# Kernel tuning notes

Measured on AMD Instinct MI355X. Metric: run time of the kernel, lower is better.

Reference implementation:

```python
import jax, jax.numpy as jnp
import numpy as np

B, T, C = 2, 2048, 4096
NH, NKV, HD = 32, 8, 128
GROUPS = NH // NKV
THETA = 10000.0


def _rope_tables(seq_len, dim, theta, dtype):
    inv_freq = 1.0 / (theta ** (jnp.arange(0, dim, 2, dtype=jnp.float32) / dim))
    t = jnp.arange(seq_len, dtype=jnp.float32)
    freqs = jnp.outer(t, inv_freq)            # [T, dim/2]
    emb = jnp.concatenate([freqs, freqs], -1)  # [T, dim]
    return jnp.cos(emb).astype(dtype), jnp.sin(emb).astype(dtype)


def _rotate_half(x):
    h = x.shape[-1] // 2
    return jnp.concatenate([-x[..., h:], x[..., :h]], axis=-1)


def setup_inputs() -> dict:
    key = jax.random.key(0)
    ks = jax.random.split(key, 5)
    s = 1.0 / np.sqrt(C)
    return {
        "x": jax.random.normal(ks[0], (B, T, C), jnp.float32),
        "wq": jax.random.normal(ks[1], (C, NH * HD), jnp.float32) * s,
        "wk": jax.random.normal(ks[2], (C, NKV * HD), jnp.float32) * s,
        "wv": jax.random.normal(ks[3], (C, NKV * HD), jnp.float32) * s,
        "wo": jax.random.normal(ks[4], (NH * HD, C), jnp.float32) * s,
    }


def reference(x, wq, wk, wv, wo):
    b, t, c = x.shape
    q = (x @ wq).reshape(b, t, NH, HD).transpose(0, 2, 1, 3)    # [B,NH,T,HD]
    k = (x @ wk).reshape(b, t, NKV, HD).transpose(0, 2, 1, 3)   # [B,NKV,T,HD]
    v = (x @ wv).reshape(b, t, NKV, HD).transpose(0, 2, 1, 3)
    cos, sin = _rope_tables(t, HD, THETA, x.dtype)              # [T,HD]
    cos = cos[None, None]
    sin = sin[None, None]
    q = q * cos + _rotate_half(q) * sin
    k = k * cos + _rotate_half(k) * sin
    # GQA: broadcast KV heads over groups via einsum instead of materializing repeat
    qg = q.reshape(b, NKV, GROUPS, t, HD)
    scores = jnp.einsum('bkgqd,bkld->bkgql', qg, k) * (HD ** -0.5)  # [B,NKV,G,T,T]
    causal = jnp.triu(jnp.full((t, t), -jnp.inf, dtype=x.dtype), k=1)
    scores = scores + causal
    attn = jax.nn.softmax(scores, axis=-1)
    out = jnp.einsum('bkgql,bkld->bkgqd', attn, v)              # [B,NKV,G,T,HD]
    out = out.reshape(b, NH, t, HD).transpose(0, 2, 1, 3).reshape(b, t, NH * HD)
    return out @ wo
```

## Files before the change

kernel.cpp:

```cpp
#include <hip/hip_runtime.h>
#include <hip/hip_bf16.h>
#include <math.h>

#define B_ 2
#define T_ 2048
#define C_ 4096
#define NH_ 32
#define NKV_ 8
#define HD_ 128
#define M_ (B_*T_)
#define QKVN_ (NH_*HD_ + 2*NKV_*HD_)

using bf16 = __hip_bfloat16;
typedef __bf16 bf16x8 __attribute__((ext_vector_type(8)));
typedef float f32x4 __attribute__((ext_vector_type(4)));

__device__ inline f32x4 mfma16(bf16x8 a, bf16x8 b, f32x4 c) {
    return __builtin_amdgcn_mfma_f32_16x16x32_bf16(a, b, c, 0, 0, 0);
}

__global__ __launch_bounds__(256) void cast_f32_bf16(const float* __restrict__ in,
                                                     bf16* __restrict__ out, int n4) {
    int i = blockIdx.x * 256 + threadIdx.x;
    if (i >= n4) return;
    float4 v = reinterpret_cast<const float4*>(in)[i];
    union { bf16 h[4]; uint2 u; } o;
    o.h[0] = __float2bfloat16(v.x);
    o.h[1] = __float2bfloat16(v.y);
    o.h[2] = __float2bfloat16(v.z);
    o.h[3] = __float2bfloat16(v.w);
    reinterpret_cast<uint2*>(out)[i] = o.u;
}

__global__ __launch_bounds__(256) void transpose_cast(const float* __restrict__ in,
                                                      bf16* __restrict__ out, int K, int N) {
    __shared__ float tile[32][33];
    int tx = threadIdx.x & 31, ty = threadIdx.x >> 5;
    int n0 = blockIdx.x << 5, k0 = blockIdx.y << 5;
#pragma unroll
    for (int p = 0; p < 4; ++p)
        tile[p*8 + ty][tx] = in[(size_t)(k0 + p*8 + ty) * N + n0 + tx];
    __syncthreads();
#pragma unroll
    for (int p = 0; p < 4; ++p)
        out[(size_t)(n0 + p*8 + ty) * K + k0 + tx] = __float2bfloat16(tile[tx][p*8 + ty]);
}

__global__ __launch_bounds__(256) void rope_tab(float2* __restrict__ tab) {
    int idx = blockIdx.x * 256 + threadIdx.x;
    int i = idx & 63, t = idx >> 6;
    float inv = exp2f((float)i * -0.20762050593045952f);
    float th = (float)t * inv;
    tab[idx] = make_float2(cosf(th), sinf(th));
}

#define GEMM_PROLOG_AND_LOOP(TAG)                                                       \
    f32x4 acc[8][4] = {};                                                               \
    bf16x8 a[4][2], b0[2][2], b1[2][2];                                                 \
    STAGE_HALF(Ag, 0,     0, 0, 0); STAGE_HALF(Ag, 0,     0, 0, 1);                     \
    STAGE_HALF(Bg, 65536, 0, 0, 0); STAGE_HALF(Bg, 65536, 0, 0, 1);                     \
    STAGE_HALF(Bg, 65536, 1, 1, 0); STAGE_HALF(Bg, 65536, 1, 1, 1);                     \
    asm volatile("s_waitcnt vmcnt(4)" ::: "memory");                                    \
    BAR();                                                                              \
    for (int it = 0; it < (nt >> 1); ++it) {                                            \
        const int u = 2 * it;                                                           \
        const bool more = (u + 2) < nt;                                                 \
        const bool more3 = (u + 3) < nt;                                                \
        READ_A(0, 0); READ_B(0, 0, b0);                                                 \
        STAGE_HALF(Ag, 0, u + 1, 1, 0);                                                 \
        MFMA_Q(0, 0, b0);                                                               \
        BAR();                                                                          \
        READ_B(0, 1, b1);                                                               \
        STAGE_HALF(Ag, 0, u + 1, 1, 1);                                                 \
        MFMA_Q(0, 2, b1);                                                               \
        BAR();                                                                          \
        READ_A(0, 1);                                                                   \
        if (more) STAGE_HALF(Bg, 65536, u + 2, 0, 0);                                   \
        MFMA_Q(4, 2, b1);                                                               \
        BAR();                                                                          \
        if (more) STAGE_HALF(Bg, 65536, u + 2, 0, 1);                                   \
        MFMA_Q(4, 0, b0);                                                               \
        if (more) asm volatile("s_waitcnt vmcnt(8)" ::: "memory");                      \
        else      asm volatile("s_waitcnt vmcnt(4)" ::: "memory");                      \
        BAR();                                                                          \
        READ_A(1, 0); READ_B(1, 0, b0);                                                 \
        if (more) STAGE_HALF(Ag, 0, u + 2, 0, 0);                                       \
        MFMA_Q(0, 0, b0);                                                               \
        BAR();                                                                          \
        READ_B(1, 1, b1);                                                               \
        if (more) STAGE_HALF(Ag, 0, u + 2, 0, 1);                                       \
        MFMA_Q(0, 2, b1);                                                               \
        if (more) asm volatile("s_waitcnt vmcnt(8)" ::: "memory");                      \
        else      asm volatile("s_waitcnt vmcnt(0)" ::: "memory");                      \
        BAR();                                                                          \
        READ_A(1, 1);                                                                   \
        if (more3) STAGE_HALF(Bg, 65536, u + 3, 1, 0);                                  \
        MFMA_Q(4, 2, b1);                                                               \
        BAR();                                                                          \
        if (more3) STAGE_HALF(Bg, 65536, u + 3, 1, 1);                                  \
        MFMA_Q(4, 0, b0);                                                               \
        if (more3) asm volatile("s_waitcnt vmcnt(4)" ::: "memory");                     \
        else       asm volatile("s_waitcnt vmcnt(0)" ::: "memory");                     \
        BAR();                                                                          \
    }

#define GEMM_COMMON_DEFS                                                                \
    __shared__ __align__(16) char lds[131072];                                          \
    const int tid = threadIdx.x;                                                        \
    const int wid = tid >> 6, lane = tid & 63;                                          \
    const int lq = lane & 15, lg = lane >> 4;                                           \
    const int wrow = wid >> 2, wcol = wid & 3;                                          \
    const int nwg = gridDim.x;                                                          \
    const int q8 = nwg >> 3;                                                            \
    const int wg = (blockIdx.x & 7) * q8 + (blockIdx.x >> 3);                           \
    const int nby = M >> 8;                                                             \
    const int by = wg % nby, bx = wg / nby;                                             \
    const int brow = by << 8, bcol = bx << 8;                                           \
    const bf16* Ag = A + (size_t)brow * K;                                              \
    const bf16* Bg = Bt + (size_t)bcol * K;                                             \
    const int nt = K >> 6;                                                              \
    const int srow = (wid << 3) + (lane >> 3);                                          \
    const int schunk = (lane & 7) ^ ((lane >> 3) & 7);

#define STAGE_HALF(gbase, ldsoff, t2, cbuf, hf)                                         \
    {                                                                                   \
        _Pragma("unroll")                                                               \
        for (int l = 0; l < 2; ++l) {                                                   \
            const int r0 = (hf) * 128 + l * 64;                                         \
            const char* src = (const char*)(gbase) +                                    \
                ((size_t)(r0 + srow) * K + (size_t)(t2) * 64) * 2 + schunk * 16;        \
            char* dst = &lds[(ldsoff) + (cbuf) * 32768 + (r0 + (wid << 3)) * 128];      \
            __builtin_amdgcn_global_load_lds(                                           \
                (const __attribute__((address_space(1))) void*)src,                     \
                (__attribute__((address_space(3))) void*)dst, 16, 0, 0);                \
        }                                                                               \
    }

#define LDA(cbuf, mh, mf, ks) \
    (*(const bf16x8*)&lds[(cbuf)*32768 + (wrow*128 + (mh)*64 + (mf)*16 + lq)*128 + ((((ks)*4 + lg)) ^ (lq & 7))*16])

#define READ_A(cbuf, mh) \
    { _Pragma("unroll") for (int mf = 0; mf < 4; ++mf) { a[mf][0] = LDA(cbuf, mh, mf, 0); a[mf][1] = LDA(cbuf, mh, mf, 1); } }
#define READ_B(cbuf, nh, breg) \
    { _Pragma("unroll") for (int nf = 0; nf < 2; ++nf) { breg[nf][0] = LDB(cbuf, nh, nf, 0); breg[nf][1] = LDB(cbuf, nh, nf, 1); } }
#define MFMA_Q(am, an, breg)                                                     \
    { __builtin_amdgcn_s_setprio(1);                                             \
      _Pragma("unroll") for (int mf = 0; mf < 4; ++mf)                           \
          _Pragma("unroll") for (int nf = 0; nf < 2; ++nf)                       \
              _Pragma("unroll") for (int ks = 0; ks < 2; ++ks)                   \
                  acc[(am) + mf][(an) + nf] = mfma16(a[mf][ks], breg[nf][ks],    \
                                                     acc[(am) + mf][(an) + nf]); \
      __builtin_amdgcn_s_setprio(0); }
#define BAR() __builtin_amdgcn_s_barrier()

__device__ inline void store_out(float* p, float v) { *p = v; }
__device__ inline void store_out(bf16*  p, float v) { *p = __float2bfloat16(v); }

template <typename OutT>
__global__ __launch_bounds__(512, 2) void gemm256(const bf16* __restrict__ A,
                                                  const bf16* __restrict__ Bt,
                                                  OutT* __restrict__ C,
                                                  int M, int N, int K) {
    GEMM_COMMON_DEFS
#define LDB(cbuf, nh, nf, ks) \
    (*(const bf16x8*)&lds[65536 + (cbuf)*32768 + (wcol*64 + (nh)*32 + (nf)*16 + lq)*128 + ((((ks)*4 + lg)) ^ (lq & 7))*16])
    GEMM_PROLOG_AND_LOOP(plain)
#undef LDB
#pragma unroll
    for (int mf = 0; mf < 8; ++mf)
#pragma unroll
        for (int nf = 0; nf < 4; ++nf)
#pragma unroll
            for (int r = 0; r < 4; ++r) {
                int row = brow + wrow * 128 + mf * 16 + lg * 4 + r;
                int col = bcol + wcol * 64 + nf * 16 + lq;
                store_out(&C[(size_t)row * N + col], acc[mf][nf][r]);
            }
}

__global__ __launch_bounds__(512, 2) void gemm_qkv(const bf16* __restrict__ A,
                                                   const bf16* __restrict__ Bt,
                                                   bf16* __restrict__ q_r,
                                                   const float2* __restrict__ tab,
                                                   int M, int K) {
    GEMM_COMMON_DEFS
#define LDB(cbuf, nh, nf, ks) \
    (*(const bf16x8*)&lds[65536 + (cbuf)*32768 + (((wcol>>1)*128 + (wcol&1)*32 + (nh)*64 + (nf)*16 + lq))*128 + ((((ks)*4 + lg)) ^ (lq & 7))*16])
    GEMM_PROLOG_AND_LOOP(remap)
#undef LDB

    const int trow = brow + wrow * 128;
    const float sc = 0.12751741230963214f;
#pragma unroll
    for (int mf = 0; mf < 8; ++mf)
#pragma unroll
        for (int j = 0; j < 2; ++j)
#pragma unroll
            for (int r = 0; r < 4; ++r) {
                int row = trow + mf*16 + lg*4 + r;
                int bb = row >> 11, tt = row & 2047;
                int i  = (wcol&1)*32 + j*16 + lq;
                float2 cs = tab[tt*64 + i];
                float x0 = acc[mf][j][r], x1 = acc[mf][j+2][r];
                float y0 = (x0*cs.x - x1*cs.y) * sc;
                float y1 = (x1*cs.x + x0*cs.y) * sc;
                int col0 = bcol + (wcol>>1)*128 + i;
                int h = col0 >> 7, hd = col0 & 127;
                bf16* dst = q_r + ((size_t)(bb*NH_ + h)*T_ + tt)*HD_;
                dst[hd]      = __float2bfloat16(y0);
                dst[hd + 64] = __float2bfloat16(y1);
            }
}

#undef GEMM_PROLOG_AND_LOOP
#undef GEMM_COMMON_DEFS
#undef STAGE_HALF
#undef LDA
#undef READ_A
#undef READ_B
#undef MFMA_Q
#undef BAR

__global__ __launch_bounds__(512, 2) void gemm_kv(const bf16* __restrict__ A,
                                                  const bf16* __restrict__ BtKV,
                                                  bf16* __restrict__ k_r,
                                                  bf16* __restrict__ vbuf,
                                                  const float2* __restrict__ tab,
                                                  int M, int K) {
    __shared__ __align__(16) char lds[98304];
    const int tid = threadIdx.x;
    const int wid = tid >> 6, lane = tid & 63;
    const int lq = lane & 15, lg = lane >> 4;
    const int wrow = wid >> 2, wcol = wid & 3;

    const int nwg = gridDim.x;
    const int q8 = nwg >> 3;
    const int wg = (blockIdx.x & 7) * q8 + (blockIdx.x >> 3);
    const int nby = M >> 7;
    const int by = wg % nby, bx = wg / nby;
    const int brow = by << 7;
    const int bcolr = bx << 8;

    const bf16* Ag = A + (size_t)brow * K;
    const bf16* Bg = BtKV + (size_t)bcolr * K;
    const int nt = K >> 6;

    const int srow = (wid << 3) + (lane >> 3);
    const int schunk = (lane & 7) ^ ((lane >> 3) & 7);

#define KV_STAGE_A(t2, cbuf, hf)                                                        \
    {                                                                                   \
        const char* src = (const char*)Ag +                                             \
            ((size_t)((hf) * 64 + srow) * K + (size_t)(t2) * 64) * 2 + schunk * 16;     \
        char* dst = &lds[(cbuf) * 16384 + ((hf) * 64 + (wid << 3)) * 128];              \
        __builtin_amdgcn_global_load_lds(                                               \
            (const __attribute__((address_space(1))) void*)src,                         \
            (__attribute__((address_space(3))) void*)dst, 16, 0, 0);                    \
    }
#define KV_STAGE_B(t2, cbuf, hf)                                                        \
    {                                                                                   \
        _Pragma("unroll")                                                               \
        for (int l = 0; l < 2; ++l) {                                                   \
            const int r0 = (hf) * 128 + l * 64;                                         \
            const char* src = (const char*)Bg +                                         \
                ((size_t)(r0 + srow) * K + (size_t)(t2) * 64) * 2 + schunk * 16;        \
            char* dst = &lds[32768 + (cbuf) * 32768 + (r0 + (wid << 3)) * 128];         \
            __builtin_amdgcn_global_load_lds(                                           \
                (const __attribute__((address_space(1))) void*)src,                     \
                (__attribute__((address_space(3))) void*)dst, 16, 0, 0);                \
        }                                                                               \
    }
#define KV_LDA(cbuf, mh, f, ks) \
    (*(const bf16x8*)&lds[(cbuf)*16384 + (wrow*64 + (mh)*32 + (f)*16 + lq)*128 + ((((ks)*4 + lg)) ^ (lq & 7))*16])
#define KV_LDB(cbuf, nh, nf, ks) \
    (*(const bf16x8*)&lds[32768 + (cbuf)*32768 + (((wcol>>1)*128 + (wcol&1)*32 + (nh)*64 + (nf)*16 + lq))*128 + ((((ks)*4 + lg)) ^ (lq & 7))*16])
#define KV_READ_A(cbuf, mh) \
    { _Pragma("unroll") for (int f = 0; f < 2; ++f) { a[f][0] = KV_LDA(cbuf, mh, f, 0); a[f][1] = KV_LDA(cbuf, mh, f, 1); } }
#define KV_READ_B(cbuf, nh, breg) \
    { _Pragma("unroll") for (int nf = 0; nf < 2; ++nf) { breg[nf][0] = KV_LDB(cbuf, nh, nf, 0); breg[nf][1] = KV_LDB(cbuf, nh, nf, 1); } }
#define KV_MFMA(am, an, breg)                                                    \
    { __builtin_amdgcn_s_setprio(1);                                             \
      _Pragma("unroll") for (int f = 0; f < 2; ++f)                              \
          _Pragma("unroll") for (int nf = 0; nf < 2; ++nf)                       \
              _Pragma("unroll") for (int ks = 0; ks < 2; ++ks)                   \
                  acc[(am) + f][(an) + nf] = mfma16(a[f][ks], breg[nf][ks],      \
                                                    acc[(am) + f][(an) + nf]);   \
      __builtin_amdgcn_s_setprio(0); }
#define KV_BAR() __builtin_amdgcn_s_barrier()

    f32x4 acc[4][4] = {};
    bf16x8 a[2][2], b0[2][2], b1[2][2];

    KV_STAGE_A(0, 0, 0); KV_STAGE_A(0, 0, 1);
    KV_STAGE_B(0, 0, 0); KV_STAGE_B(0, 0, 1);
    KV_STAGE_B(1, 1, 0); KV_STAGE_B(1, 1, 1);
    asm volatile("s_waitcnt vmcnt(4)" ::: "memory");
    KV_BAR();

    for (int it = 0; it < (nt >> 1); ++it) {
        const int u = 2 * it;
        const bool more = (u + 2) < nt;
        const bool more3 = (u + 3) < nt;

        KV_READ_A(0, 0); KV_READ_B(0, 0, b0);
        KV_STAGE_A(u + 1, 1, 0);
        KV_MFMA(0, 0, b0);
        KV_BAR();
        KV_READ_B(0, 1, b1);
        KV_STAGE_A(u + 1, 1, 1);
        KV_MFMA(0, 2, b1);
        KV_BAR();
        KV_READ_A(0, 1);
        if (more) KV_STAGE_B(u + 2, 0, 0);
        KV_MFMA(2, 2, b1);
        KV_BAR();
        if (more) KV_STAGE_B(u + 2, 0, 1);
        KV_MFMA(2, 0, b0);
        if (more) asm volatile("s_waitcnt vmcnt(4)" ::: "memory");
        else      asm volatile("s_waitcnt vmcnt(0)" ::: "memory");
        KV_BAR();
        KV_READ_A(1, 0); KV_READ_B(1, 0, b0);
        if (more) KV_STAGE_A(u + 2, 0, 0);
        KV_MFMA(0, 0, b0);
        KV_BAR();
        KV_READ_B(1, 1, b1);
        if (more) KV_STAGE_A(u + 2, 0, 1);
        KV_MFMA(0, 2, b1);
        KV_BAR();
        KV_READ_A(1, 1);
        if (more3) KV_STAGE_B(u + 3, 1, 0);
        KV_MFMA(2, 2, b1);
        KV_BAR();
        if (more3) KV_STAGE_B(u + 3, 1, 1);
        KV_MFMA(2, 0, b0);
        if (more3) asm volatile("s_waitcnt vmcnt(4)" ::: "memory");
        else       asm volatile("s_waitcnt vmcnt(0)" ::: "memory");
        KV_BAR();
    }

    const int trow = brow + wrow * 64;
    if (bcolr >= 1024) {
#pragma unroll
        for (int mf = 0; mf < 4; ++mf)
#pragma unroll
            for (int j = 0; j < 4; ++j)
#pragma unroll
                for (int r = 0; r < 4; ++r) {
                    int row = trow + (mf>>1)*32 + (mf&1)*16 + lg*4 + r;
                    int col = bcolr + (wcol>>1)*128 + (wcol&1)*32 + (j>>1)*64 + (j&1)*16 + lq - 1024;
                    vbuf[(size_t)row * (NKV_*HD_) + col] = __float2bfloat16(acc[mf][j][r]);
                }
    } else {
#pragma unroll
        for (int mf = 0; mf < 4; ++mf)
#pragma unroll
            for (int j = 0; j < 2; ++j)
#pragma unroll
                for (int r = 0; r < 4; ++r) {
                    int row = trow + (mf>>1)*32 + (mf&1)*16 + lg*4 + r;
                    int bb = row >> 11, tt = row & 2047;
                    int i  = (wcol&1)*32 + j*16 + lq;
                    float2 cs = tab[tt*64 + i];
                    float x0 = acc[mf][j][r], x1 = acc[mf][j+2][r];
                    float y0 = x0*cs.x - x1*cs.y;
                    float y1 = x1*cs.x + x0*cs.y;
                    int col0 = bcolr + (wcol>>1)*128 + i;
                    int h = col0 >> 7, hd = col0 & 127;
                    bf16* dst = k_r + ((size_t)(bb*NKV_ + h)*T_ + tt)*HD_;
                    dst[hd]      = __float2bfloat16(y0);
                    dst[hd + 64] = __float2bfloat16(y1);
                }
    }
#undef KV_STAGE_A
#undef KV_STAGE_B
#undef KV_LDA
#undef KV_LDB
#undef KV_READ_A
#undef KV_READ_B
#undef KV_MFMA
#undef KV_BAR
}

__global__ __launch_bounds__(256) void vtrans(const bf16* __restrict__ vbuf,
                                              bf16* __restrict__ vt) {
    __shared__ bf16 tile[32][33];
    int gx = blockIdx.x;
    int dt = gx & 3;
    int tt = (gx >> 2) & 63;
    int kv = (gx >> 8) & 7;
    int b  = gx >> 11;
    int d0 = dt * 32, t0 = tt * 32;
    int tx = threadIdx.x & 31, ty = threadIdx.x >> 5;

    const bf16* src = vbuf + (size_t)(b * T_ + t0) * (NKV_*HD_) + kv * HD_ + d0;
#pragma unroll
    for (int p = 0; p < 4; ++p)
        tile[p*8 + ty][tx] = src[(size_t)(p*8 + ty) * (NKV_*HD_) + tx];
    __syncthreads();
    bf16* dst = vt + ((size_t)((b * NKV_ + kv) * HD_ + d0)) * T_ + t0;
#pragma unroll
    for (int p = 0; p < 4; ++p)
        dst[(size_t)(p*8 + ty) * T_ + tx] = tile[tx][p*8 + ty];
}

__global__ __launch_bounds__(1024) void fattn(const bf16* __restrict__ Q,
                                              const bf16* __restrict__ Kt,
                                              const bf16* __restrict__ VT,
                                              bf16* __restrict__ O) {
    const int lin = blockIdx.x;
    const int kv = lin & 7;
    const int b  = (lin >> 3) & 1;
    const int idx = lin >> 4;
    const int h  = kv * 4 + (idx & 3);
    const int jp = idx >> 2;

    const int tid = threadIdx.x, wid = tid >> 6, lane = tid & 63;
    const int lq = lane & 15, lg = lane >> 4;

    const bf16* Kp = Kt + (size_t)(b * NKV_ + kv) * T_ * HD_;
    const bf16* Vp = VT + (size_t)(b * NKV_ + kv) * HD_ * T_;

    __shared__ __align__(16) bf16 Ks[2][64][128];
    __shared__ __align__(16) bf16 Vs[2][128][64];
    __shared__ __align__(16) bf16 p_lds[16][16][72];

    const float THR_L2 = 11.5416f;

#define STAGE_KV(cbuf, tt)                                                           \
    { {                                                                              \
        int krow = wid * 4 + (lane >> 4);                                            \
        int kch  = (lane & 15) ^ (krow & 15);                                        \
        const bf16* ksrc = Kp + (size_t)((tt) * 64 + krow) * HD_ + kch * 8;          \
        __builtin_amdgcn_global_load_lds(                                            \
            (const __attribute__((address_space(1))) void*)ksrc,                     \
            (__attribute__((address_space(3))) void*)&Ks[cbuf][wid*4][0],            \
            16, 0, 0);                                                               \
      }                                                                              \
      {                                                                              \
        int vrow = wid * 8 + (lane >> 3);                                            \
        int vch  = (lane & 7) ^ (vrow & 7);                                          \
        const bf16* vsrc = Vp + (size_t)vrow * T_ + (tt) * 64 + vch * 8;             \
        __builtin_amdgcn_global_load_lds(                                            \
            (const __attribute__((address_space(1))) void*)vsrc,                     \
            (__attribute__((address_space(3))) void*)&Vs[cbuf][wid*8][0],            \
            16, 0, 0);                                                               \
      } }

    for (int half = 0; half < 2; ++half) {
        const int qt = half ? (7 - jp) : jp;
        const int q0 = qt * 256 + wid * 16;
        const int kv_end = q0 + 16;
        const int NT = qt * 4 + 4;

        const bf16* Qp = Q + ((size_t)(b * NH_ + h) * T_ + q0) * HD_;
        bf16x8 qf[4];
#pragma unroll
        for (int c = 0; c < 4; ++c)
            qf[c] = *(const bf16x8*)&Qp[(size_t)lq * HD_ + c * 32 + lg * 8];

        f32x4 oacc[8] = {};
        float m_r = -INFINITY;
        float l_r = 0.f;

        STAGE_KV(0, 0);
        STAGE_KV(1, 1);
        asm volatile("s_waitcnt vmcnt(2)" ::: "memory");
        __builtin_amdgcn_s_barrier();

        for (int t = 0; t < NT; ++t) {
            const int cb = t & 1;
            const int t0 = t * 64;

            if (t0 < kv_end) {
                f32x4 st[4] = {};
#pragma unroll
                for (int n = 0; n < 4; ++n) {
                    bf16x8 kf[4];
#pragma unroll
                    for (int c = 0; c < 4; ++c)
                        kf[c] = *(const bf16x8*)((const char*)&Ks[cb][n*16 + lq][0]
                                                  + (((c*4 + lg) ^ lq) << 4));
                    __builtin_amdgcn_s_setprio(1);
#pragma unroll
                    for (int c = 0; c < 4; ++c)
                        st[n] = mfma16(kf[c], qf[c], st[n]);
                    __builtin_amdgcn_s_setprio(0);
                }

                const int qq = q0 + lq;
#pragma unroll
                for (int n = 0; n < 4; ++n)
#pragma unroll
                    for (int r = 0; r < 4; ++r) {
                        int kk = t0 + n*16 + lg*4 + r;
                        if (kk > qq) st[n][r] = -INFINITY;
                    }

                float rmax = st[0][0];
#pragma unroll
                for (int n = 0; n < 4; ++n)
#pragma unroll
                    for (int r = 0; r < 4; ++r) rmax = fmaxf(rmax, st[n][r]);
                rmax = fmaxf(rmax, __shfl_xor(rmax, 16));
                rmax = fmaxf(rmax, __shfl_xor(rmax, 32));

                if (__any(rmax - m_r > THR_L2)) {
                    float mnew = fmaxf(m_r, rmax);
                    float alpha = exp2f(m_r - mnew);
                    m_r = mnew;
                    l_r *= alpha;
#pragma unroll
                    for (int r = 0; r < 4; ++r) {
                        float a_pv = __shfl(alpha, lg*4 + r);
#pragma unroll
                        for (int f = 0; f < 8; ++f) oacc[f][r] *= a_pv;
                    }
                }

                float rsum = 0.f;
#pragma unroll
                for (int n = 0; n < 4; ++n)
#pragma unroll
                    for (int r = 0; r < 4; ++r) {
                        float p = exp2f(st[n][r] - m_r);
                        st[n][r] = p;
                        rsum += p;
                    }
                rsum += __shfl_xor(rsum, 16);
                rsum += __shfl_xor(rsum, 32);
                l_r += rsum;

#pragma unroll
                for (int n = 0; n < 4; ++n) {
                    union { bf16 hh[4]; uint2 u; } pk;
#pragma unroll
                    for (int r = 0; r < 4; ++r) pk.hh[r] = __float2bfloat16(st[n][r]);
                    *(uint2*)&p_lds[wid][lq][n*16 + lg*4] = pk.u;
                }

#pragma unroll
                for (int ks = 0; ks < 2; ++ks) {
                    bf16x8 pa = *(const bf16x8*)&p_lds[wid][lq][ks*32 + lg*8];
                    bf16x8 vf[8];
#pragma unroll
                    for (int f = 0; f < 8; ++f)
                        vf[f] = *(const bf16x8*)((const char*)&Vs[cb][f*16 + lq][0]
                                                  + (((ks*4 + lg) ^ (lq & 7)) << 4));
                    __builtin_amdgcn_s_setprio(1);
#pragma unroll
                    for (int f = 0; f < 8; ++f)
                        oacc[f] = mfma16(pa, vf[f], oacc[f]);
                    __builtin_amdgcn_s_setprio(0);
                }
            }

            __builtin_amdgcn_s_barrier();
            if (t + 2 < NT) {
                STAGE_KV(cb, t + 2);
                asm volatile("s_waitcnt vmcnt(2)" ::: "memory");
            } else {
                asm volatile("s_waitcnt vmcnt(0)" ::: "memory");
            }
            __builtin_amdgcn_s_barrier();
        }

        {
            float rinv = __builtin_amdgcn_rcpf(l_r);
#pragma unroll
            for (int r = 0; r < 4; ++r) {
                float rl = __shfl(rinv, lg*4 + r);
                int row = q0 + lg*4 + r;
#pragma unroll
                for (int f = 0; f < 8; ++f) {
                    int d = f*16 + lq;
                    O[((size_t)(b * T_ + row) * NH_ + h) * HD_ + d] =
                        __float2bfloat16(oacc[f][r] * rl);
                }
            }
        }
    }
#undef STAGE_KV
}

extern "C" void kernel_launch(void* const* d_in, const int* in_sizes, int n_in,
                              void* d_out, int out_size, void* d_ws, size_t ws_size,
                              hipStream_t stream) {
    const float* x  = (const float*)d_in[0];
    const float* wq = (const float*)d_in[1];
    const float* wk = (const float*)d_in[2];
    const float* wv = (const float*)d_in[3];
    const float* wo = (const float*)d_in[4];
    float* out = (float*)d_out;

    bf16* ws    = (bf16*)d_ws;
    bf16* xb    = ws;
    bf16* wqkvT = xb + (size_t)M_ * C_;
    bf16* qr_wo = wqkvT + (size_t)QKVN_ * C_;
    bf16* region = qr_wo + (size_t)C_ * C_;
    bf16* k_r  = region;
    bf16* vt   = k_r + (size_t)B_ * NKV_ * T_ * HD_;
    bf16* vbuf = vt  + (size_t)B_ * NKV_ * T_ * HD_;
    float2* tab = (float2*)(vbuf + (size_t)B_ * T_ * NKV_ * HD_);

    bf16* attn = xb;

    cast_f32_bf16<<<(M_ * C_ / 4 + 255) / 256, 256, 0, stream>>>(x, xb, M_ * C_ / 4);
    transpose_cast<<<dim3(128, 128), 256, 0, stream>>>(wq, wqkvT, C_, NH_ * HD_);
    transpose_cast<<<dim3(32, 128), 256, 0, stream>>>(wk, wqkvT + (size_t)(NH_ * HD_) * C_, C_, NKV_ * HD_);
    transpose_cast<<<dim3(32, 128), 256, 0, stream>>>(wv, wqkvT + (size_t)(NH_ * HD_ + NKV_ * HD_) * C_, C_, NKV_ * HD_);
    rope_tab<<<(T_ * 64) / 256, 256, 0, stream>>>(tab);

    gemm_qkv<<<dim3((C_ / 256) * (M_ / 256)), 512, 0, stream>>>(
        xb, wqkvT, qr_wo, tab, M_, C_);
    gemm_kv<<<dim3(256), 512, 0, stream>>>(
        xb, wqkvT + (size_t)(NH_ * HD_) * C_, k_r, vbuf, tab, M_, C_);

    vtrans<<<B_ * NKV_ * (T_ / 32) * (HD_ / 32), 256, 0, stream>>>(vbuf, vt);

    fattn<<<dim3(256), 1024, 0, stream>>>(qr_wo, k_r, vt, attn);

    transpose_cast<<<dim3(128, 128), 256, 0, stream>>>(wo, qr_wo, NH_ * HD_, C_);
    gemm256<float><<<dim3((C_ / 256) * (M_ / 256)), 512, 0, stream>>>(attn, qr_wo, out, M_, C_, C_);
}
```

Measured before the change: 478.1 us.

## Merge Q and KV projection GEMMs into one kernel and fuse weight transposes

Combines the three QKV weight transpose-cast launches into a single kernel that picks the source matrix by block index. Also fuses the Q projection GEMM and the KV projection GEMM into one 256-block kernel where each workgroup first computes a Q tile, then a KV tile, sharing one LDS allocation. This removes launch overhead and the tail/idle gap between the two GEMMs, at the cost of serializing both tiles per block and a fixed grid size that must match both tilings.

After: 471.5 us. About the same (-1.4%).

```diff
diff --git a/kernel.cpp b/kernel.cpp
--- a/kernel.cpp
+++ b/kernel.cpp
@@ -44,6 +44,27 @@
 #pragma unroll
     for (int p = 0; p < 4; ++p)
         out[(size_t)(n0 + p*8 + ty) * K + k0 + tx] = __float2bfloat16(tile[tx][p*8 + ty]);
+}
+
+__global__ __launch_bounds__(256) void transpose_cast3(const float* __restrict__ wq,
+                                                       const float* __restrict__ wk,
+                                                       const float* __restrict__ wv,
+                                                       bf16* __restrict__ out, int K) {
+    __shared__ float tile[32][33];
+    int tx = threadIdx.x & 31, ty = threadIdx.x >> 5;
+    int nt = blockIdx.x, k0 = blockIdx.y << 5;
+    const float* src; int N, nloc;
+    if (nt < 128)      { src = wq; N = 4096; nloc = nt << 5; }
+    else if (nt < 160) { src = wk; N = 1024; nloc = (nt - 128) << 5; }
+    else               { src = wv; N = 1024; nloc = (nt - 160) << 5; }
+#pragma unroll
+    for (int p = 0; p < 4; ++p)
+        tile[p*8 + ty][tx] = src[(size_t)(k0 + p*8 + ty) * N + nloc + tx];
+    __syncthreads();
+    int nglob = nt << 5;
+#pragma unroll
+    for (int p = 0; p < 4; ++p)
+        out[(size_t)(nglob + p*8 + ty) * K + k0 + tx] = __float2bfloat16(tile[tx][p*8 + ty]);
 }
 
 __global__ __launch_bounds__(256) void rope_tab(float2* __restrict__ tab) {
@@ -105,7 +126,6 @@
     }
 
 #define GEMM_COMMON_DEFS                                                                \
-    __shared__ __align__(16) char lds[131072];                                          \
     const int tid = threadIdx.x;                                                        \
     const int wid = tid >> 6, lane = tid & 63;                                          \
     const int lq = lane & 15, lg = lane >> 4;                                           \
@@ -113,12 +133,6 @@
     const int nwg = gridDim.x;                                                          \
     const int q8 = nwg >> 3;                                                            \
     const int wg = (blockIdx.x & 7) * q8 + (blockIdx.x >> 3);                           \
-    const int nby = M >> 8;                                                             \
-    const int by = wg % nby, bx = wg / nby;                                             \
-    const int brow = by << 8, bcol = bx << 8;                                           \
-    const bf16* Ag = A + (size_t)brow * K;                                              \
-    const bf16* Bg = Bt + (size_t)bcol * K;                                             \
-    const int nt = K >> 6;                                                              \
     const int srow = (wid << 3) + (lane >> 3);                                          \
     const int schunk = (lane & 7) ^ ((lane >> 3) & 7);
 
@@ -161,7 +175,14 @@
                                                   const bf16* __restrict__ Bt,
                                                   OutT* __restrict__ C,
                                                   int M, int N, int K) {
+    __shared__ __align__(16) char lds[131072];
     GEMM_COMMON_DEFS
+    const int nby = M >> 8;
+    const int by = wg % nby, bx = wg / nby;
+    const int brow = by << 8, bcol = bx << 8;
+    const bf16* Ag = A + (size_t)brow * K;
+    const bf16* Bg = Bt + (size_t)bcol * K;
+    const int nt = K >> 6;
 #define LDB(cbuf, nh, nf, ks) \
     (*(const bf16x8*)&lds[65536 + (cbuf)*32768 + (wcol*64 + (nh)*32 + (nf)*16 + lq)*128 + ((((ks)*4 + lg)) ^ (lq & 7))*16])
     GEMM_PROLOG_AND_LOOP(plain)
@@ -178,75 +199,59 @@
             }
 }
 
-__global__ __launch_bounds__(512, 2) void gemm_qkv(const bf16* __restrict__ A,
-                                                   const bf16* __restrict__ Bt,
-                                                   bf16* __restrict__ q_r,
-                                                   const float2* __restrict__ tab,
-                                                   int M, int K) {
+__global__ __launch_bounds__(512, 2) void gemm_qkv_all(const bf16* __restrict__ A,
+                                                       const bf16* __restrict__ Bt,
+                                                       bf16* __restrict__ q_r,
+                                                       bf16* __restrict__ k_r,
+                                                       bf16* __restrict__ vbuf,
+                                                       const float2* __restrict__ tab,
+                                                       int M, int K) {
+    __shared__ __align__(16) char lds[131072];
     GEMM_COMMON_DEFS
+
+    {
+        const int nby = M >> 8;
+        const int by = wg % nby, bx = wg / nby;
+        const int brow = by << 8, bcol = bx << 8;
+        const bf16* Ag = A + (size_t)brow * K;
+        const bf16* Bg = Bt + (size_t)bcol * K;
+        const int nt = K >> 6;
 #define LDB(cbuf, nh, nf, ks) \
     (*(const bf16x8*)&lds[65536 + (cbuf)*32768 + (((wcol>>1)*128 + (wcol&1)*32 + (nh)*64 + (nf)*16 + lq))*128 + ((((ks)*4 + lg)) ^ (lq & 7))*16])
-    GEMM_PROLOG_AND_LOOP(remap)
+        GEMM_PROLOG_AND_LOOP(remap)
 #undef LDB
-
-    const int trow = brow + wrow * 128;
-    const float sc = 0.12751741230963214f;
-#pragma unroll
-    for (int mf = 0; mf < 8; ++mf)
-#pragma unroll
-        for (int j = 0; j < 2; ++j)
-#pragma unroll
-            for (int r = 0; r < 4; ++r) {
-                int row = trow + mf*16 + lg*4 + r;
-                int bb = row >> 11, tt = row & 2047;
-                int i  = (wcol&1)*32 + j*16 + lq;
-                float2 cs = tab[tt*64 + i];
-                float x0 = acc[mf][j][r], x1 = acc[mf][j+2][r];
-                float y0 = (x0*cs.x - x1*cs.y) * sc;
-                float y1 = (x1*cs.x + x0*cs.y) * sc;
-                int col0 = bcol + (wcol>>1)*128 + i;
-                int h = col0 >> 7, hd = col0 & 127;
-                bf16* dst = q_r + ((size_t)(bb*NH_ + h)*T_ + tt)*HD_;
-                dst[hd]      = __float2bfloat16(y0);
-                dst[hd + 64] = __float2bfloat16(y1);
-            }
-}
-
-#undef GEMM_PROLOG_AND_LOOP
-#undef GEMM_COMMON_DEFS
-#undef STAGE_HALF
-#undef LDA
-#undef READ_A
-#undef READ_B
-#undef MFMA_Q
-#undef BAR
-
-__global__ __launch_bounds__(512, 2) void gemm_kv(const bf16* __restrict__ A,
-                                                  const bf16* __restrict__ BtKV,
-                                                  bf16* __restrict__ k_r,
-                                                  bf16* __restrict__ vbuf,
-                                                  const float2* __restrict__ tab,
-                                                  int M, int K) {
-    __shared__ __align__(16) char lds[98304];
-    const int tid = threadIdx.x;
-    const int wid = tid >> 6, lane = tid & 63;
-    const int lq = lane & 15, lg = lane >> 4;
-    const int wrow = wid >> 2, wcol = wid & 3;
-
-    const int nwg = gridDim.x;
-    const int q8 = nwg >> 3;
-    const int wg = (blockIdx.x & 7) * q8 + (blockIdx.x >> 3);
-    const int nby = M >> 7;
-    const int by = wg % nby, bx = wg / nby;
-    const int brow = by << 7;
-    const int bcolr = bx << 8;
-
-    const bf16* Ag = A + (size_t)brow * K;
-    const bf16* Bg = BtKV + (size_t)bcolr * K;
-    const int nt = K >> 6;
-
-    const int srow = (wid << 3) + (lane >> 3);
-    const int schunk = (lane & 7) ^ ((lane >> 3) & 7);
+        const int trow = brow + wrow * 128;
+        const float sc = 0.12751741230963214f;
+#pragma unroll
+        for (int mf = 0; mf < 8; ++mf)
+#pragma unroll
+            for (int j = 0; j < 2; ++j)
+#pragma unroll
+                for (int r = 0; r < 4; ++r) {
+                    int row = trow + mf*16 + lg*4 + r;
+                    int bb = row >> 11, tt = row & 2047;
+                    int i  = (wcol&1)*32 + j*16 + lq;
+                    float2 cs = tab[tt*64 + i];
+                    float x0 = acc[mf][j][r], x1 = acc[mf][j+2][r];
+                    float y0 = (x0*cs.x - x1*cs.y) * sc;
+                    float y1 = (x1*cs.x + x0*cs.y) * sc;
+                    int col0 = bcol + (wcol>>1)*128 + i;
+                    int h = col0 >> 7, hd = col0 & 127;
+                    bf16* dst = q_r + ((size_t)(bb*NH_ + h)*T_ + tt)*HD_;
+                    dst[hd]      = __float2bfloat16(y0);
+                    dst[hd + 64] = __float2bfloat16(y1);
+                }
+    }
+    __builtin_amdgcn_s_barrier();
+
+    {
+        const int nby = M >> 7;
+        const int by = wg % nby, bx = wg / nby;
+        const int brow = by << 7;
+        const int bcolr = bx << 8;
+        const bf16* Ag = A + (size_t)brow * K;
+        const bf16* Bg = Bt + ((size_t)(NH_*HD_) + bcolr) * K;
+        const int nt = K >> 6;
 
 #define KV_STAGE_A(t2, cbuf, hf)                                                        \
     {                                                                                   \
@@ -286,91 +291,90 @@
                   acc[(am) + f][(an) + nf] = mfma16(a[f][ks], breg[nf][ks],      \
                                                     acc[(am) + f][(an) + nf]);   \
       __builtin_amdgcn_s_setprio(0); }
-#define KV_BAR() __builtin_amdgcn_s_barrier()
-
-    f32x4 acc[4][4] = {};
-    bf16x8 a[2][2], b0[2][2], b1[2][2];
-
-    KV_STAGE_A(0, 0, 0); KV_STAGE_A(0, 0, 1);
-    KV_STAGE_B(0, 0, 0); KV_STAGE_B(0, 0, 1);
-    KV_STAGE_B(1, 1, 0); KV_STAGE_B(1, 1, 1);
-    asm volatile("s_waitcnt vmcnt(4)" ::: "memory");
-    KV_BAR();
-
-    for (int it = 0; it < (nt >> 1); ++it) {
-        const int u = 2 * it;
-        const bool more = (u + 2) < nt;
-        const bool more3 = (u + 3) < nt;
-
-        KV_READ_A(0, 0); KV_READ_B(0, 0, b0);
-        KV_STAGE_A(u + 1, 1, 0);
-        KV_MFMA(0, 0, b0);
-        KV_BAR();
-        KV_READ_B(0, 1, b1);
-        KV_STAGE_A(u + 1, 1, 1);
-        KV_MFMA(0, 2, b1);
-        KV_BAR();
-        KV_READ_A(0, 1);
-        if (more) KV_STAGE_B(u + 2, 0, 0);
-        KV_MFMA(2, 2, b1);
-        KV_BAR();
-        if (more) KV_STAGE_B(u + 2, 0, 1);
-        KV_MFMA(2, 0, b0);
-        if (more) asm volatile("s_waitcnt vmcnt(4)" ::: "memory");
-        else      asm volatile("s_waitcnt vmcnt(0)" ::: "memory");
-        KV_BAR();
-        KV_READ_A(1, 0); KV_READ_B(1, 0, b0);
-        if (more) KV_STAGE_A(u + 2, 0, 0);
-        KV_MFMA(0, 0, b0);
-        KV_BAR();
-        KV_READ_B(1, 1, b1);
-        if (more) KV_STAGE_A(u + 2, 0, 1);
-        KV_MFMA(0, 2, b1);
-        KV_BAR();
-        KV_READ_A(1, 1);
-        if (more3) KV_STAGE_B(u + 3, 1, 0);
-        KV_MFMA(2, 2, b1);
-        KV_BAR();
-        if (more3) KV_STAGE_B(u + 3, 1, 1);
-        KV_MFMA(2, 0, b0);
-        if (more3) asm volatile("s_waitcnt vmcnt(4)" ::: "memory");
-        else       asm volatile("s_waitcnt vmcnt(0)" ::: "memory");
-        KV_BAR();
-    }
-
-    const int trow = brow + wrow * 64;
-    if (bcolr >= 1024) {
-#pragma unroll
-        for (int mf = 0; mf < 4; ++mf)
-#pragma unroll
-            for (int j = 0; j < 4; ++j)
-#pragma unroll
-                for (int r = 0; r < 4; ++r) {
-                    int row = trow + (mf>>1)*32 + (mf&1)*16 + lg*4 + r;
-                    int col = bcolr + (wcol>>1)*128 + (wcol&1)*32 + (j>>1)*64 + (j&1)*16 + lq - 1024;
-                    vbuf[(size_t)row * (NKV_*HD_) + col] = __float2bfloat16(acc[mf][j][r]);
-                }
-    } else {
-#pragma unroll
-        for (int mf = 0; mf < 4; ++mf)
-#pragma unroll
-            for (int j = 0; j < 2; ++j)
-#pragma unroll
-                for (int r = 0; r < 4; ++r) {
-                    int row = trow + (mf>>1)*32 + (mf&1)*16 + lg*4 + r;
-                    int bb = row >> 11, tt = row & 2047;
-                    int i  = (wcol&1)*32 + j*16 + lq;
-                    float2 cs = tab[tt*64 + i];
-                    float x0 = acc[mf][j][r], x1 = acc[mf][j+2][r];
-                    float y0 = x0*cs.x - x1*cs.y;
-                    float y1 = x1*cs.x + x0*cs.y;
-                    int col0 = bcolr + (wcol>>1)*128 + i;
-                    int h = col0 >> 7, hd = col0 & 127;
-                    bf16* dst = k_r + ((size_t)(bb*NKV_ + h)*T_ + tt)*HD_;
-                    dst[hd]      = __float2bfloat16(y0);
-                    dst[hd + 64] = __float2bfloat16(y1);
-                }
-    }
+
+        f32x4 acc[4][4] = {};
+        bf16x8 a[2][2], b0[2][2], b1[2][2];
+
+        KV_STAGE_A(0, 0, 0); KV_STAGE_A(0, 0, 1);
+        KV_STAGE_B(0, 0, 0); KV_STAGE_B(0, 0, 1);
+        KV_STAGE_B(1, 1, 0); KV_STAGE_B(1, 1, 1);
+        asm volatile("s_waitcnt vmcnt(4)" ::: "memory");
+        BAR();
+
+        for (int it = 0; it < (nt >> 1); ++it) {
+            const int u = 2 * it;
+            const bool more = (u + 2) < nt;
+            const bool more3 = (u + 3) < nt;
+
+            KV_READ_A(0, 0); KV_READ_B(0, 0, b0);
+            KV_STAGE_A(u + 1, 1, 0);
+            KV_MFMA(0, 0, b0);
+            BAR();
+            KV_READ_B(0, 1, b1);
+            KV_STAGE_A(u + 1, 1, 1);
+            KV_MFMA(0, 2, b1);
+            BAR();
+            KV_READ_A(0, 1);
+            if (more) KV_STAGE_B(u + 2, 0, 0);
+            KV_MFMA(2, 2, b1);
+            BAR();
+            if (more) KV_STAGE_B(u + 2, 0, 1);
+            KV_MFMA(2, 0, b0);
+            if (more) asm volatile("s_waitcnt vmcnt(4)" ::: "memory");
+            else      asm volatile("s_waitcnt vmcnt(0)" ::: "memory");
+            BAR();
+            KV_READ_A(1, 0); KV_READ_B(1, 0, b0);
+            if (more) KV_STAGE_A(u + 2, 0, 0);
+            KV_MFMA(0, 0, b0);
+            BAR();
+            KV_READ_B(1, 1, b1);
+            if (more) KV_STAGE_A(u + 2, 0, 1);
+            KV_MFMA(0, 2, b1);
+            BAR();
+            KV_READ_A(1, 1);
+            if (more3) KV_STAGE_B(u + 3, 1, 0);
+            KV_MFMA(2, 2, b1);
+            BAR();
+            if (more3) KV_STAGE_B(u + 3, 1, 1);
+            KV_MFMA(2, 0, b0);
+            if (more3) asm volatile("s_waitcnt vmcnt(4)" ::: "memory");
+            else       asm volatile("s_waitcnt vmcnt(0)" ::: "memory");
+            BAR();
+        }
+
+        const int trow = brow + wrow * 64;
+        if (bcolr >= 1024) {
+#pragma unroll
+            for (int mf = 0; mf < 4; ++mf)
+#pragma unroll
+                for (int j = 0; j < 4; ++j)
+#pragma unroll
+                    for (int r = 0; r < 4; ++r) {
+                        int row = trow + (mf>>1)*32 + (mf&1)*16 + lg*4 + r;
+                        int col = bcolr + (wcol>>1)*128 + (wcol&1)*32 + (j>>1)*64 + (j&1)*16 + lq - 1024;
+                        vbuf[(size_t)row * (NKV_*HD_) + col] = __float2bfloat16(acc[mf][j][r]);
+                    }
+        } else {
+#pragma unroll
+            for (int mf = 0; mf < 4; ++mf)
+#pragma unroll
+                for (int j = 0; j < 2; ++j)
+#pragma unroll
+                    for (int r = 0; r < 4; ++r) {
+                        int row = trow + (mf>>1)*32 + (mf&1)*16 + lg*4 + r;
+                        int bb = row >> 11, tt = row & 2047;
+                        int i  = (wcol&1)*32 + j*16 + lq;
+                        float2 cs = tab[tt*64 + i];
+                        float x0 = acc[mf][j][r], x1 = acc[mf][j+2][r];
+                        float y0 = x0*cs.x - x1*cs.y;
+                        float y1 = x1*cs.x + x0*cs.y;
+                        int col0 = bcolr + (wcol>>1)*128 + i;
+                        int h = col0 >> 7, hd = col0 & 127;
+                        bf16* dst = k_r + ((size_t)(bb*NKV_ + h)*T_ + tt)*HD_;
+                        dst[hd]      = __float2bfloat16(y0);
+                        dst[hd + 64] = __float2bfloat16(y1);
+                    }
+        }
 #undef KV_STAGE_A
 #undef KV_STAGE_B
 #undef KV_LDA
@@ -378,8 +382,17 @@
 #undef KV_READ_A
 #undef KV_READ_B
 #undef KV_MFMA
-#undef KV_BAR
-}
+    }
+}
+
+#undef GEMM_PROLOG_AND_LOOP
+#undef GEMM_COMMON_DEFS
+#undef STAGE_HALF
+#undef LDA
+#undef READ_A
+#undef READ_B
+#undef MFMA_Q
+#undef BAR
 
 __global__ __launch_bounds__(256) void vtrans(const bf16* __restrict__ vbuf,
                                               bf16* __restrict__ vt) {
@@ -605,15 +618,11 @@
     bf16* attn = xb;
 
     cast_f32_bf16<<<(M_ * C_ / 4 + 255) / 256, 256, 0, stream>>>(x, xb, M_ * C_ / 4);
-    transpose_cast<<<dim3(128, 128), 256, 0, stream>>>(wq, wqkvT, C_, NH_ * HD_);
-    transpose_cast<<<dim3(32, 128), 256, 0, stream>>>(wk, wqkvT + (size_t)(NH_ * HD_) * C_, C_, NKV_ * HD_);
-    transpose_cast<<<dim3(32, 128), 256, 0, stream>>>(wv, wqkvT + (size_t)(NH_ * HD_ + NKV_ * HD_) * C_, C_, NKV_ * HD_);
+    transpose_cast3<<<dim3(192, 128), 256, 0, stream>>>(wq, wk, wv, wqkvT, C_);
     rope_tab<<<(T_ * 64) / 256, 256, 0, stream>>>(tab);
 
-    gemm_qkv<<<dim3((C_ / 256) * (M_ / 256)), 512, 0, stream>>>(
-        xb, wqkvT, qr_wo, tab, M_, C_);
-    gemm_kv<<<dim3(256), 512, 0, stream>>>(
-        xb, wqkvT + (size_t)(NH_ * HD_) * C_, k_r, vbuf, tab, M_, C_);
+    gemm_qkv_all<<<dim3(256), 512, 0, stream>>>(
+        xb, wqkvT, qr_wo, k_r, vbuf, tab, M_, C_);
 
     vtrans<<<B_ * NKV_ * (T_ / 32) * (HD_ / 32), 256, 0, stream>>>(vbuf, vt);
 
```
